# Kernel tuning notes

Hardware: AMD Instinct MI355X
Metric: run time of the kernel (lower is better)

## Reference

```python
import jax, jax.numpy as jnp
import numpy as np

B = 1024
NUM_DENSE = 13
NUM_SPARSE = 26
VOCAB = 100000
EMB_DIM = 16
BOT = [512, 256, 64, 16]
TOP = [1024, 512, 256]
D_INT = BOT[-1] + NUM_SPARSE * EMB_DIM  # 432
OUT_INT = D_INT * (D_INT + 1) // 2      # 93528


def setup_inputs() -> dict:
    key = jax.random.key(0)
    ks = jax.random.split(key, 32)
    inp = {
        "dense_features": jax.random.normal(ks[0], (B, NUM_DENSE), jnp.float32),
        "sparse_features": jax.random.randint(ks[1], (B, NUM_SPARSE), 0, VOCAB),
        "emb_tables": jax.random.normal(ks[2], (NUM_SPARSE, VOCAB, EMB_DIM), jnp.float32) * 0.02,
    }
    # bottom MLP weights (in, out) convention
    dims = [NUM_DENSE] + BOT
    for i in range(len(BOT)):
        inp[f"bw{i}"] = jax.random.normal(ks[3 + i], (dims[i], dims[i + 1]), jnp.float32) * 0.02
        inp[f"bb{i}"] = jnp.zeros((dims[i + 1],), jnp.float32)
    tdims = [BOT[-1] + OUT_INT] + TOP + [1]
    for i in range(len(TOP) + 1):
        inp[f"tw{i}"] = jax.random.normal(ks[10 + i], (tdims[i], tdims[i + 1]), jnp.float32) * 0.02
        inp[f"tb{i}"] = jnp.zeros((tdims[i + 1],), jnp.float32)
    return inp


def _forward(dense_features, emb_tables, bws, bbs, tws, tbs, sparse_features):
    # bottom MLP: Linear+ReLU stacks
    h = dense_features
    for w, b in zip(bws, bbs):
        h = jax.nn.relu(h @ w + b)
    dense_out = h  # (B, 16)
    # embedding lookups: table t indexed by column t of sparse_features
    # emb_tables: (F, V, E); gather per-table then flatten -> (B, F*E)
    emb = jnp.take_along_axis(
        emb_tables[None],  # (1, F, V, E)
        sparse_features.T[None, :, :, None].transpose(0, 1, 2, 3) * 0 + sparse_features.T[None, :, :, None],
        axis=2,
    )  # placeholder avoided below
    # cleaner: vmap over tables
    emb = jax.vmap(lambda tbl, idx: tbl[idx], in_axes=(0, 1))(emb_tables, sparse_features)  # (F, B, E)
    emb = jnp.transpose(emb, (1, 0, 2)).reshape(dense_features.shape[0], -1)  # (B, F*E)
    x = jnp.concatenate([dense_out, emb], axis=1)  # (B, D_INT)
    # pairwise interaction: upper triangle (incl. diagonal) of outer product.
    iu0, iu1 = np.triu_indices(x.shape[1])
    inter = x[:, iu0] * x[:, iu1]  # (B, OUT_INT) -- only needed entries
    z = jnp.concatenate([dense_out, inter], axis=1)
    n_top = len(tws)
    for i, (w, b) in enumerate(zip(tws, tbs)):
        z = z @ w + b
        if i < n_top - 1:
            z = jax.nn.relu(z)
    return z


def reference(dense_features, sparse_features, emb_tables,
              bw0, bb0, bw1, bb1, bw2, bb2, bw3, bb3,
              tw0, tb0, tw1, tb1, tw2, tb2, tw3, tb3):
    bws = [bw0, bw1, bw2, bw3]
    bbs = [bb0, bb1, bb2, bb3]
    tws = [tw0, tw1, tw2, tw3]
    tbs = [tb0, tb1, tb2, tb3]
    return _forward(dense_features, emb_tables, bws, bbs, tws, tbs, sparse_features)
```

## Files before the change

### kernel.cpp

```cpp
#include <hip/hip_runtime.h>
#include <stdint.h>

typedef unsigned short ushort_t;
typedef __attribute__((ext_vector_type(4))) float f32x4;
typedef __attribute__((ext_vector_type(8))) short s16x8;

#define DEVFN static __device__ __forceinline__

constexpr int B_   = 1024;
constexpr int P_   = 93528;
constexpr int K1   = 93544;
constexpr int Kp   = 94208;
constexpr int SPLITS = 16;
constexpr int KCH  = Kp / SPLITS;
constexpr int KSTEPS = KCH / 64;

DEVFN ushort_t f2bf(float f) {
  union { float f; unsigned int u; } x; x.f = f;
  unsigned int r = x.u + 0x7FFFu + ((x.u >> 16) & 1u);
  return (ushort_t)(r >> 16);
}

DEVFN void gload_lds16(const void* g, void* l) {
  __builtin_amdgcn_global_load_lds((const __attribute__((address_space(1))) unsigned int*)g,
                                   (__attribute__((address_space(3))) unsigned int*)l, 16, 0, 0);
}

__global__ __launch_bounds__(256) void k_pre(const float* __restrict__ dense,
    const int* __restrict__ sparse, const float* __restrict__ tbl,
    const float* __restrict__ bw0, const float* __restrict__ bb0,
    const float* __restrict__ bw1, const float* __restrict__ bb1,
    const float* __restrict__ bw2, const float* __restrict__ bb2,
    const float* __restrict__ bw3, const float* __restrict__ bb3,
    int* __restrict__ iu, float* __restrict__ xT) {
  __shared__ float sm[13520];
  int bid = blockIdx.x, t = threadIdx.x;
  if (bid < 368) {
    int k = bid * 256 + t;
    if (bid < 8) {
      int idx = bid * 256 + t;
      xT[432 * 1024 + idx] = (idx < 1024) ? 1.f : 0.f;
    }
    if (k >= Kp) return;
    int v;
    if (k < 16) v = k | (432 << 16);
    else if (k >= K1) v = 433 | (433 << 16);
    else {
      int p = k - 16;
      float s = sqrtf((float)(748225 - 8 * p));
      int i = (int)((865.0f - s) * 0.5f);
      if (i < 0) i = 0; if (i > 431) i = 431;
      while (i < 431 && (i + 1) * (865 - (i + 1)) / 2 <= p) ++i;
      while (i > 0 && i * (865 - i) / 2 > p) --i;
      int j = i + (p - i * (865 - i) / 2);
      v = i | (j << 16);
    }
    iu[k] = v;
  } else if (bid < 432) {
    float* xs = sm;
    float* h1 = sm + 208;
    float* h2 = h1 + 8192;
    float* h3 = h2 + 4096;
    int m0 = (bid - 368) * 16;
    if (t < 208) xs[t] = dense[m0 * 13 + t];
    __syncthreads();
    #pragma unroll
    for (int h = 0; h < 2; ++h) {
      int n = h * 256 + t;
      float a[16];
      float bv = bb0[n];
      #pragma unroll
      for (int r = 0; r < 16; ++r) a[r] = bv;
      for (int k = 0; k < 13; ++k) {
        float w = bw0[k * 512 + n];
        #pragma unroll
        for (int r = 0; r < 16; ++r) a[r] = fmaf(xs[r * 13 + k], w, a[r]);
      }
      #pragma unroll
      for (int r = 0; r < 16; ++r) h1[r * 512 + n] = fmaxf(a[r], 0.f);
    }
    __syncthreads();
    {
      int n = t;
      float a[16];
      float bv = bb1[n];
      #pragma unroll
      for (int r = 0; r < 16; ++r) a[r] = bv;
      for (int k = 0; k < 512; ++k) {
        float w = bw1[k * 256 + n];
        #pragma unroll
        for (int r = 0; r < 16; ++r) a[r] = fmaf(h1[r * 512 + k], w, a[r]);
      }
      #pragma unroll
      for (int r = 0; r < 16; ++r) h2[r * 256 + n] = fmaxf(a[r], 0.f);
    }
    __syncthreads();
    {
      int n = t & 63, r0 = t >> 6;
      float a[4];
      float bv = bb2[n];
      #pragma unroll
      for (int i = 0; i < 4; ++i) a[i] = bv;
      for (int k = 0; k < 256; ++k) {
        float w = bw2[k * 64 + n];
        #pragma unroll
        for (int i = 0; i < 4; ++i) a[i] = fmaf(h2[(r0 + 4 * i) * 256 + k], w, a[i]);
      }
      #pragma unroll
      for (int i = 0; i < 4; ++i) h3[(r0 + 4 * i) * 64 + n] = fmaxf(a[i], 0.f);
    }
    __syncthreads();
    {
      int n = t & 15, r = t >> 4;
      float a = bb3[n];
      for (int k = 0; k < 64; ++k) a = fmaf(h3[r * 64 + k], bw3[k * 16 + n], a);
      xT[(size_t)n * B_ + m0 + r] = fmaxf(a, 0.f);
    }
  } else {
    int e = bid - 432;
    int f = e >> 2;
    int b = (e & 3) * 256 + t;
    int idx = sparse[(size_t)b * 26 + f];
    const float4* src = (const float4*)(tbl + ((size_t)f * 100000 + idx) * 16);
    #pragma unroll
    for (int q = 0; q < 4; ++q) {
      float4 v = src[q];
      int r = 16 + f * 16 + q * 4;
      xT[(size_t)(r + 0) * B_ + b] = v.x;
      xT[(size_t)(r + 1) * B_ + b] = v.y;
      xT[(size_t)(r + 2) * B_ + b] = v.z;
      xT[(size_t)(r + 3) * B_ + b] = v.w;
    }
  }
}

__global__ __launch_bounds__(256, 8) void k_gz(const float* __restrict__ xT,
                                               const int* __restrict__ iu,
                                               const float* __restrict__ tw0,
                                               ushort_t* __restrict__ Z,
                                               ushort_t* __restrict__ WT) {
  __shared__ int ls_iu[512];
  int bid = blockIdx.x, t = threadIdx.x;
  int r3 = bid % 3;
  if (r3 == 0) {
    int idx = bid / 3;
    int l = t & 63, w = t >> 6;
    int mb = (idx & 15) * 64;
    int kt = (idx >> 4) * 512;
    ls_iu[t] = iu[kt + t];
    ls_iu[256 + t] = iu[kt + 256 + t];
    __syncthreads();
    uint32_t moff = mb + l;
    int kw = w * 128;
    #pragma unroll 2
    for (int g = 0; g < 16; ++g) {
      int kloc = kw + g * 8;
      int4 ij0 = *(const int4*)&ls_iu[kloc];
      int4 ij1 = *(const int4*)&ls_iu[kloc + 4];
      float p[8];
      {
        int v0 = ij0.x, v1 = ij0.y, v2 = ij0.z, v3 = ij0.w;
        p[0] = xT[(uint32_t)((v0 & 0xFFFF) << 10) + moff] * xT[(uint32_t)((v0 >> 16) << 10) + moff];
        p[1] = xT[(uint32_t)((v1 & 0xFFFF) << 10) + moff] * xT[(uint32_t)((v1 >> 16) << 10) + moff];
        p[2] = xT[(uint32_t)((v2 & 0xFFFF) << 10) + moff] * xT[(uint32_t)((v2 >> 16) << 10) + moff];
        p[3] = xT[(uint32_t)((v3 & 0xFFFF) << 10) + moff] * xT[(uint32_t)((v3 >> 16) << 10) + moff];
        v0 = ij1.x; v1 = ij1.y; v2 = ij1.z; v3 = ij1.w;
        p[4] = xT[(uint32_t)((v0 & 0xFFFF) << 10) + moff] * xT[(uint32_t)((v0 >> 16) << 10) + moff];
        p[5] = xT[(uint32_t)((v1 & 0xFFFF) << 10) + moff] * xT[(uint32_t)((v1 >> 16) << 10) + moff];
        p[6] = xT[(uint32_t)((v2 & 0xFFFF) << 10) + moff] * xT[(uint32_t)((v2 >> 16) << 10) + moff];
        p[7] = xT[(uint32_t)((v3 & 0xFFFF) << 10) + moff] * xT[(uint32_t)((v3 >> 16) << 10) + moff];
      }
      union { uint32_t w4[4]; int4 v4; } o;
      asm("v_cvt_pk_bf16_f32 %0, %1, %2" : "=v"(o.w4[0]) : "v"(p[0]), "v"(p[1]));
      asm("v_cvt_pk_bf16_f32 %0, %1, %2" : "=v"(o.w4[1]) : "v"(p[2]), "v"(p[3]));
      asm("v_cvt_pk_bf16_f32 %0, %1, %2" : "=v"(o.w4[2]) : "v"(p[4]), "v"(p[5]));
      asm("v_cvt_pk_bf16_f32 %0, %1, %2" : "=v"(o.w4[3]) : "v"(p[6]), "v"(p[7]));
      int kglob = kt + kloc;
      *(int4*)&Z[((size_t)(kglob >> 3) * 1024 + moff) * 8] = o.v4;
    }
  } else {
    int idx = (bid / 3) * 2 + r3 - 1;
    int k0 = (idx % 368) * 256, n0 = (idx / 368) * 64;
    int nl = t & 63, kq = t >> 6;
    int n = n0 + nl;
    int kbase = k0 + kq * 64;
    const float* src = tw0 + (size_t)kbase * 1024 + n;
    ushort_t* dst = WT + ((size_t)(kbase >> 3) * 1024 + n) * 8;
    bool full = (kbase + 64 <= K1);
    #pragma unroll
    for (int g = 0; g < 8; ++g) {
      float v[8];
      if (full) {
        #pragma unroll
        for (int e = 0; e < 8; ++e) v[e] = src[(size_t)(g * 8 + e) << 10];
      } else {
        #pragma unroll
        for (int e = 0; e < 8; ++e) {
          int k = kbase + g * 8 + e;
          v[e] = (k < K1) ? src[(size_t)(g * 8 + e) << 10] : 0.f;
        }
      }
      union { uint32_t w4[4]; int4 v4; } o;
      asm("v_cvt_pk_bf16_f32 %0, %1, %2" : "=v"(o.w4[0]) : "v"(v[0]), "v"(v[1]));
      asm("v_cvt_pk_bf16_f32 %0, %1, %2" : "=v"(o.w4[1]) : "v"(v[2]), "v"(v[3]));
      asm("v_cvt_pk_bf16_f32 %0, %1, %2" : "=v"(o.w4[2]) : "v"(v[4]), "v"(v[5]));
      asm("v_cvt_pk_bf16_f32 %0, %1, %2" : "=v"(o.w4[3]) : "v"(v[6]), "v"(v[7]));
      *(int4*)(dst + (size_t)g * 8192) = o.v4;
    }
  }
}

__global__ __launch_bounds__(512, 2) void k_gemm(const ushort_t* __restrict__ Z,
                                                 const ushort_t* __restrict__ WT,
                                                 float* __restrict__ part) {
  __shared__ ushort_t lds[65536];
  int t = threadIdx.x;
  int bid = blockIdx.x;
  int x = bid & 7, r = bid >> 3;
  int g = (x << 3) | (r & 7);
  int s = g >> 2;
  int m0 = (g & 3) * 256, n0 = (r >> 3) * 256;
  int kb = s * KCH;

  int rr = t >> 3, cc = t & 7;
  int cs = cc ^ (rr & 7);
  const ushort_t* pa0 = Z  + (((size_t)(kb >> 3) + cs) * 1024 + m0 + rr) * 8;
  const ushort_t* pb0 = WT + (((size_t)(kb >> 3) + cs) * 1024 + n0 + rr) * 8;
  int l0 = t * 8;

  int w = t >> 6, l = t & 63;
  int wm = (w >> 2) * 128, wn = (w & 3) * 64;
  int lhi = l >> 4, llo = l & 15;

  f32x4 acc[8][4];
  #pragma unroll
  for (int a = 0; a < 8; ++a)
    #pragma unroll
    for (int b = 0; b < 4; ++b) acc[a][b] = f32x4{0.f, 0.f, 0.f, 0.f};

  s16x8 bf[4][2], afX[4], afY[4];

  auto rdA = [&](s16x8* dst, int mfb, const ushort_t* Ab) {
    #pragma unroll
    for (int j = 0; j < 2; ++j)
      #pragma unroll
      for (int ks = 0; ks < 2; ++ks) {
        int row = wm + (mfb + j) * 16 + llo;
        int ch = (ks * 4 + lhi) ^ (row & 7);
        dst[j * 2 + ks] = *(const s16x8*)&Ab[row * 64 + ch * 8];
      }
  };
  auto rdB = [&](const ushort_t* Bb) {
    #pragma unroll
    for (int nf = 0; nf < 4; ++nf)
      #pragma unroll
      for (int ks = 0; ks < 2; ++ks) {
        int row = wn + nf * 16 + llo;
        int ch = (ks * 4 + lhi) ^ (row & 7);
        bf[nf][ks] = *(const s16x8*)&Bb[row * 64 + ch * 8];
      }
  };

#define MFMA_PHASE(P, AF)                                                        \
  __builtin_amdgcn_s_barrier();                                                  \
  asm volatile("s_waitcnt lgkmcnt(0)" ::: "memory");                             \
  __builtin_amdgcn_sched_barrier(0);                                             \
  __builtin_amdgcn_s_setprio(1);                                                 \
  _Pragma("unroll")                                                              \
  for (int j = 0; j < 2; ++j)                                                    \
    _Pragma("unroll")                                                            \
    for (int nf = 0; nf < 4; ++nf)                                               \
      _Pragma("unroll")                                                          \
      for (int ks = 0; ks < 2; ++ks)                                             \
        acc[(P) * 2 + j][nf] = __builtin_amdgcn_mfma_f32_16x16x32_bf16(          \
            AF[j * 2 + ks], bf[nf][ks], acc[(P) * 2 + j][nf], 0, 0, 0);          \
  __builtin_amdgcn_s_setprio(0);                                                 \
  __builtin_amdgcn_sched_barrier(0);                                             \
  __builtin_amdgcn_s_barrier();

  #pragma unroll
  for (int i = 0; i < 4; ++i) gload_lds16(pa0 + i * 512, &lds[i * 4096 + l0]);
  #pragma unroll
  for (int i = 0; i < 4; ++i) gload_lds16(pb0 + i * 512, &lds[32768 + i * 4096 + l0]);
  #pragma unroll
  for (int i = 0; i < 4; ++i) gload_lds16(pb0 + 65536 + i * 512, &lds[32768 + 16384 + i * 4096 + l0]);
  asm volatile("s_waitcnt vmcnt(4)" ::: "memory");
  __builtin_amdgcn_s_barrier();
  rdA(afX, 0, &lds[0]);

  for (int tt = 0; tt < KSTEPS; ++tt) {
    const ushort_t* Ab = &lds[(tt & 1) * 16384];
    const ushort_t* An = &lds[((tt + 1) & 1) * 16384];
    const ushort_t* Bb = &lds[32768 + (tt & 1) * 16384];
    ushort_t* dA  = &lds[((tt + 1) & 1) * 16384];
    ushort_t* dB2 = &lds[32768 + (tt & 1) * 16384];
    const ushort_t* sA  = pa0 + (size_t)(tt + 1) * 65536;
    const ushort_t* sB2 = pb0 + (size_t)(tt + 2) * 65536;
    bool pf1 = (tt + 1 < KSTEPS);
    bool pf2 = (tt + 2 < KSTEPS);

    rdB(Bb);
    rdA(afY, 2, Ab);
    if (pf1) {
      gload_lds16(sA,       dA + l0);
      gload_lds16(sA + 512, dA + 4096 + l0);
    }
    MFMA_PHASE(0, afX)

    rdA(afX, 4, Ab);
    if (pf1) {
      gload_lds16(sA + 1024, dA + 2 * 4096 + l0);
      gload_lds16(sA + 1536, dA + 3 * 4096 + l0);
    }
    MFMA_PHASE(1, afY)

    rdA(afY, 6, Ab);
    if (pf2) {
      gload_lds16(sB2,       dB2 + l0);
      gload_lds16(sB2 + 512, dB2 + 4096 + l0);
    }
    MFMA_PHASE(2, afX)

    if (pf1) {
      if (pf2) asm volatile("s_waitcnt vmcnt(2)" ::: "memory");
      else     asm volatile("s_waitcnt vmcnt(0)" ::: "memory");
      rdA(afX, 0, An);
    }
    if (pf2) {
      gload_lds16(sB2 + 1024, dB2 + 2 * 4096 + l0);
      gload_lds16(sB2 + 1536, dB2 + 3 * 4096 + l0);
    }
    MFMA_PHASE(3, afY)
  }
#undef MFMA_PHASE

  float* pbase = part + ((size_t)s << 20);
  #pragma unroll
  for (int mf = 0; mf < 8; ++mf)
    #pragma unroll
    for (int nf = 0; nf < 4; ++nf) {
      int n = n0 + wn + nf * 16 + llo;
      #pragma unroll
      for (int r2 = 0; r2 < 4; ++r2) {
        int m = m0 + wm + mf * 16 + lhi * 4 + r2;
        pbase[(size_t)m * 1024 + n] = acc[mf][nf][r2];
      }
    }
}

__global__ __launch_bounds__(256) void k_red(const float* __restrict__ part,
                                             const float* __restrict__ bias,
                                             float* __restrict__ z1) {
  int idx = blockIdx.x * 256 + threadIdx.x;
  float a = bias[idx & 1023];
  #pragma unroll
  for (int s = 0; s < SPLITS; ++s) a += part[((size_t)s << 20) + idx];
  z1[idx] = fmaxf(a, 0.f);
}

template<int K, int N>
__global__ __launch_bounds__(256) void k_sgemm(const float* __restrict__ A,
                                               const float* __restrict__ W,
                                               const float* __restrict__ bias,
                                               float* __restrict__ C) {
  __shared__ float As[16][34];
  __shared__ float Bs[16][68];
  int t = threadIdx.x;
  int m0 = blockIdx.x * 32, n0 = blockIdx.y * 64;
  int tx = t & 15, ty = t >> 4;
  float acc[2][4];
  #pragma unroll
  for (int j = 0; j < 2; ++j)
    #pragma unroll
    for (int q = 0; q < 4; ++q) acc[j][q] = 0.f;
  int ar = t >> 3, ak = (t & 7) * 2;
  int bk = t >> 4, bn = (t & 15) * 4;
  for (int k0 = 0; k0 < K; k0 += 16) {
    float2 av = *(const float2*)&A[(size_t)(m0 + ar) * K + k0 + ak];
    float4 bv = *(const float4*)&W[(size_t)(k0 + bk) * N + n0 + bn];
    __syncthreads();
    As[ak][ar] = av.x; As[ak + 1][ar] = av.y;
    *(float4*)&Bs[bk][bn] = bv;
    __syncthreads();
    #pragma unroll
    for (int k = 0; k < 16; ++k) {
      float2 a = *(const float2*)&As[k][ty * 2];
      float4 b = *(const float4*)&Bs[k][tx * 4];
      acc[0][0] = fmaf(a.x, b.x, acc[0][0]); acc[0][1] = fmaf(a.x, b.y, acc[0][1]);
      acc[0][2] = fmaf(a.x, b.z, acc[0][2]); acc[0][3] = fmaf(a.x, b.w, acc[0][3]);
      acc[1][0] = fmaf(a.y, b.x, acc[1][0]); acc[1][1] = fmaf(a.y, b.y, acc[1][1]);
      acc[1][2] = fmaf(a.y, b.z, acc[1][2]); acc[1][3] = fmaf(a.y, b.w, acc[1][3]);
    }
  }
  #pragma unroll
  for (int j = 0; j < 2; ++j) {
    int m = m0 + ty * 2 + j;
    float4 o;
    o.x = fmaxf(acc[j][0] + bias[n0 + tx * 4 + 0], 0.f);
    o.y = fmaxf(acc[j][1] + bias[n0 + tx * 4 + 1], 0.f);
    o.z = fmaxf(acc[j][2] + bias[n0 + tx * 4 + 2], 0.f);
    o.w = fmaxf(acc[j][3] + bias[n0 + tx * 4 + 3], 0.f);
    *(float4*)&C[(size_t)m * N + n0 + tx * 4] = o;
  }
}

__global__ __launch_bounds__(256) void k_last(const float* __restrict__ z3,
                                              const float* __restrict__ w,
                                              const float* __restrict__ bias,
                                              float* __restrict__ out) {
  int t = threadIdx.x, l = t & 63, wv = t >> 6;
  int m = blockIdx.x * 4 + wv;
  float s = 0.f;
  #pragma unroll
  for (int c = 0; c < 4; ++c) s = fmaf(z3[(size_t)m * 256 + c * 64 + l], w[c * 64 + l], s);
  #pragma unroll
  for (int off = 32; off; off >>= 1) s += __shfl_down(s, off, 64);
  if (l == 0) out[m] = s + bias[0];
}

__global__ __launch_bounds__(256) void k_z1init(const float* __restrict__ bias, float* __restrict__ z1) {
  int idx = blockIdx.x * 256 + threadIdx.x;
  z1[idx] = bias[idx & 1023];
}
__global__ __launch_bounds__(256) void k_relu(float* __restrict__ z1) {
  int idx = blockIdx.x * 256 + threadIdx.x;
  z1[idx] = fmaxf(z1[idx], 0.f);
}
constexpr int FB_S = 8;
__global__ __launch_bounds__(256) void k_fbgemm(const float* __restrict__ xT,
                                                const int* __restrict__ iu,
                                                const float* __restrict__ tw0,
                                                float* __restrict__ z1) {
  __shared__ float zs[32 * 64];
  __shared__ float wsb[32 * 64];
  int t = threadIdx.x;
  int m0 = blockIdx.x * 64, n0 = blockIdx.y * 64, s = blockIdx.z;
  int kch = (K1 + FB_S - 1) / FB_S;
  int k0 = s * kch, kend = min(k0 + kch, K1);
  float acc[16];
  #pragma unroll
  for (int q = 0; q < 16; ++q) acc[q] = 0.f;
  int mm = t & 63, ng = t >> 6;
  for (int kk = k0; kk < kend; kk += 32) {
    __syncthreads();
    for (int sl = t; sl < 2048; sl += 256) {
      int kloc = sl >> 6, v6 = sl & 63;
      int k = kk + kloc;
      float zv = 0.f, wv = 0.f;
      if (k < kend) {
        int ij = iu[k];
        int i = ij & 0xFFFF, j = ij >> 16;
        zv = xT[(size_t)i * B_ + m0 + v6] * xT[(size_t)j * B_ + m0 + v6];
        wv = tw0[(size_t)k * 1024 + n0 + v6];
      }
      zs[kloc * 64 + v6] = zv;
      wsb[kloc * 64 + v6] = wv;
    }
    __syncthreads();
    #pragma unroll 4
    for (int kloc = 0; kloc < 32; ++kloc) {
      float zv = zs[kloc * 64 + mm];
      #pragma unroll
      for (int q = 0; q < 16; ++q)
        acc[q] = fmaf(zv, wsb[kloc * 64 + ng * 16 + q], acc[q]);
    }
  }
  #pragma unroll
  for (int q = 0; q < 16; ++q)
    atomicAdd(&z1[(size_t)(m0 + mm) * 1024 + n0 + ng * 16 + q], acc[q]);
}

extern "C" void kernel_launch(void* const* d_in, const int* in_sizes, int n_in,
                              void* d_out, int out_size, void* d_ws, size_t ws_size,
                              hipStream_t stream) {
  const float* dense  = (const float*)d_in[0];
  const int*   sparse = (const int*)  d_in[1];
  const float* emb    = (const float*)d_in[2];
  const float* bw0 = (const float*)d_in[3];  const float* bb0 = (const float*)d_in[4];
  const float* bw1 = (const float*)d_in[5];  const float* bb1 = (const float*)d_in[6];
  const float* bw2 = (const float*)d_in[7];  const float* bb2 = (const float*)d_in[8];
  const float* bw3 = (const float*)d_in[9];  const float* bb3 = (const float*)d_in[10];
  const float* tw0 = (const float*)d_in[11]; const float* tb0 = (const float*)d_in[12];
  const float* tw1 = (const float*)d_in[13]; const float* tb1 = (const float*)d_in[14];
  const float* tw2 = (const float*)d_in[15]; const float* tb2 = (const float*)d_in[16];
  const float* tw3 = (const float*)d_in[17]; const float* tb3 = (const float*)d_in[18];
  float* out = (float*)d_out;

  char* ws = (char*)d_ws;
  size_t off = 0;
  auto alloc = [&](size_t bytes) -> char* {
    char* p = ws + off;
    off = (off + bytes + 255) & ~(size_t)255;
    return p;
  };
  float* xT = (float*)alloc((size_t)434 * 1024 * 4);
  int*   iu = (int*)  alloc((size_t)Kp * 4);
  float* z1 = (float*)alloc((size_t)1024 * 1024 * 4);
  float* z2 = (float*)alloc((size_t)1024 * 512 * 4);
  float* z3 = (float*)alloc((size_t)1024 * 256 * 4);
  ushort_t* Z    = (ushort_t*)alloc((size_t)1024 * Kp * 2);
  ushort_t* WT   = (ushort_t*)alloc((size_t)1024 * Kp * 2);
  float*    part = (float*)   alloc((size_t)SPLITS * 1024 * 1024 * 4);
  bool big = (off <= ws_size);

  k_pre<<<536, 256, 0, stream>>>(dense, sparse, emb, bw0, bb0, bw1, bb1, bw2, bb2, bw3, bb3, iu, xT);

  if (big) {
    k_gz<<<8832, 256, 0, stream>>>(xT, iu, tw0, Z, WT);
    k_gemm<<<256, 512, 0, stream>>>(Z, WT, part);
    k_red<<<4096, 256, 0, stream>>>(part, tb0, z1);
  } else {
    k_z1init<<<4096, 256, 0, stream>>>(tb0, z1);
    k_fbgemm<<<dim3(16, 16, FB_S), 256, 0, stream>>>(xT, iu, tw0, z1);
    k_relu<<<4096, 256, 0, stream>>>(z1);
  }

  k_sgemm<1024, 512><<<dim3(32, 8), 256, 0, stream>>>(z1, tw1, tb1, z2);
  k_sgemm<512, 256><<<dim3(32, 4), 256, 0, stream>>>(z2, tw2, tb2, z3);
  k_last<<<256, 256, 0, stream>>>(z3, tw3, tb3, out);
}
```

Measured before the change: 530.3 us.

## Move tw0 bf16 conversion into pre kernel and split bottom MLP finer

The fp32-to-bf16 transposed conversion of tw0 moves from the Z-generation kernel into the preprocessing kernel, because it depends only on weights. It then runs alongside the bottom MLP, embedding gather and index-table work, and Z generation becomes its own smaller kernel. The bottom MLP now uses 256 blocks of 4 rows each instead of 64 blocks of 16, which spreads that long serial chain across more CUs and shrinks shared memory. In exchange the pre kernel gets a very large grid that mixes heterogeneous work, and the MLP blocks reread the weights more often.

```diff
diff --git a/kernel.cpp b/kernel.cpp
--- a/kernel.cpp
+++ b/kernel.cpp
@@ -32,13 +32,70 @@
     const float* __restrict__ bw1, const float* __restrict__ bb1,
     const float* __restrict__ bw2, const float* __restrict__ bb2,
     const float* __restrict__ bw3, const float* __restrict__ bb3,
-    int* __restrict__ iu, float* __restrict__ xT) {
-  __shared__ float sm[13520];
+    const float* __restrict__ tw0,
+    int* __restrict__ iu, float* __restrict__ xT, ushort_t* __restrict__ WT) {
+  __shared__ float sm[3392];
   int bid = blockIdx.x, t = threadIdx.x;
-  if (bid < 368) {
-    int k = bid * 256 + t;
-    if (bid < 8) {
-      int idx = bid * 256 + t;
+  if (bid < 256) {
+    float* xs = sm;
+    float* h1 = sm + 64;
+    float* h2 = h1 + 2048;
+    float* h3 = h2 + 1024;
+    int m0 = bid * 4;
+    if (t < 52) xs[t] = dense[m0 * 13 + t];
+    __syncthreads();
+    #pragma unroll
+    for (int h = 0; h < 2; ++h) {
+      int n = h * 256 + t;
+      float a[4];
+      float bv = bb0[n];
+      #pragma unroll
+      for (int r = 0; r < 4; ++r) a[r] = bv;
+      for (int k = 0; k < 13; ++k) {
+        float w = bw0[k * 512 + n];
+        #pragma unroll
+        for (int r = 0; r < 4; ++r) a[r] = fmaf(xs[r * 13 + k], w, a[r]);
+      }
+      #pragma unroll
+      for (int r = 0; r < 4; ++r) h1[r * 512 + n] = fmaxf(a[r], 0.f);
+    }
+    __syncthreads();
+    {
+      int n = t;
+      float a[4];
+      float bv = bb1[n];
+      #pragma unroll
+      for (int r = 0; r < 4; ++r) a[r] = bv;
+      #pragma unroll 8
+      for (int k = 0; k < 512; ++k) {
+        float w = bw1[k * 256 + n];
+        #pragma unroll
+        for (int r = 0; r < 4; ++r) a[r] = fmaf(h1[r * 512 + k], w, a[r]);
+      }
+      #pragma unroll
+      for (int r = 0; r < 4; ++r) h2[r * 256 + n] = fmaxf(a[r], 0.f);
+    }
+    __syncthreads();
+    {
+      int n = t & 63, r = t >> 6;
+      float a = bb2[n];
+      #pragma unroll 8
+      for (int k = 0; k < 256; ++k) a = fmaf(h2[r * 256 + k], bw2[k * 64 + n], a);
+      h3[r * 64 + n] = fmaxf(a, 0.f);
+    }
+    __syncthreads();
+    if (t < 64) {
+      int n = t & 15, r = t >> 4;
+      float a = bb3[n];
+      #pragma unroll 8
+      for (int k = 0; k < 64; ++k) a = fmaf(h3[r * 64 + k], bw3[k * 16 + n], a);
+      xT[(size_t)n * B_ + m0 + r] = fmaxf(a, 0.f);
+    }
+  } else if (bid < 624) {
+    int bb = bid - 256;
+    int k = bb * 256 + t;
+    if (bb < 8) {
+      int idx = bb * 256 + t;
       xT[432 * 1024 + idx] = (idx < 1024) ? 1.f : 0.f;
     }
     if (k >= Kp) return;
@@ -56,68 +113,8 @@
       v = i | (j << 16);
     }
     iu[k] = v;
-  } else if (bid < 432) {
-    float* xs = sm;
-    float* h1 = sm + 208;
-    float* h2 = h1 + 8192;
-    float* h3 = h2 + 4096;
-    int m0 = (bid - 368) * 16;
-    if (t < 208) xs[t] = dense[m0 * 13 + t];
-    __syncthreads();
-    #pragma unroll
-    for (int h = 0; h < 2; ++h) {
-      int n = h * 256 + t;
-      float a[16];
-      float bv = bb0[n];
-      #pragma unroll
-      for (int r = 0; r < 16; ++r) a[r] = bv;
-      for (int k = 0; k < 13; ++k) {
-        float w = bw0[k * 512 + n];
-        #pragma unroll
-        for (int r = 0; r < 16; ++r) a[r] = fmaf(xs[r * 13 + k], w, a[r]);
-      }
-      #pragma unroll
-      for (int r = 0; r < 16; ++r) h1[r * 512 + n] = fmaxf(a[r], 0.f);
-    }
-    __syncthreads();
-    {
-      int n = t;
-      float a[16];
-      float bv = bb1[n];
-      #pragma unroll
-      for (int r = 0; r < 16; ++r) a[r] = bv;
-      for (int k = 0; k < 512; ++k) {
-        float w = bw1[k * 256 + n];
-        #pragma unroll
-        for (int r = 0; r < 16; ++r) a[r] = fmaf(h1[r * 512 + k], w, a[r]);
-      }
-      #pragma unroll
-      for (int r = 0; r < 16; ++r) h2[r * 256 + n] = fmaxf(a[r], 0.f);
-    }
-    __syncthreads();
-    {
-      int n = t & 63, r0 = t >> 6;
-      float a[4];
-      float bv = bb2[n];
-      #pragma unroll
-      for (int i = 0; i < 4; ++i) a[i] = bv;
-      for (int k = 0; k < 256; ++k) {
-        float w = bw2[k * 64 + n];
-        #pragma unroll
-        for (int i = 0; i < 4; ++i) a[i] = fmaf(h2[(r0 + 4 * i) * 256 + k], w, a[i]);
-      }
-      #pragma unroll
-      for (int i = 0; i < 4; ++i) h3[(r0 + 4 * i) * 64 + n] = fmaxf(a[i], 0.f);
-    }
-    __syncthreads();
-    {
-      int n = t & 15, r = t >> 4;
-      float a = bb3[n];
-      for (int k = 0; k < 64; ++k) a = fmaf(h3[r * 64 + k], bw3[k * 16 + n], a);
-      xT[(size_t)n * B_ + m0 + r] = fmaxf(a, 0.f);
-    }
-  } else {
-    int e = bid - 432;
+  } else if (bid < 728) {
+    int e = bid - 624;
     int f = e >> 2;
     int b = (e & 3) * 256 + t;
     int idx = sparse[(size_t)b * 26 + f];
@@ -131,55 +128,8 @@
       xT[(size_t)(r + 2) * B_ + b] = v.z;
       xT[(size_t)(r + 3) * B_ + b] = v.w;
     }
-  }
-}
-
-__global__ __launch_bounds__(256, 8) void k_gz(const float* __restrict__ xT,
-                                               const int* __restrict__ iu,
-                                               const float* __restrict__ tw0,
-                                               ushort_t* __restrict__ Z,
-                                               ushort_t* __restrict__ WT) {
-  __shared__ int ls_iu[512];
-  int bid = blockIdx.x, t = threadIdx.x;
-  int r3 = bid % 3;
-  if (r3 == 0) {
-    int idx = bid / 3;
-    int l = t & 63, w = t >> 6;
-    int mb = (idx & 15) * 64;
-    int kt = (idx >> 4) * 512;
-    ls_iu[t] = iu[kt + t];
-    ls_iu[256 + t] = iu[kt + 256 + t];
-    __syncthreads();
-    uint32_t moff = mb + l;
-    int kw = w * 128;
-    #pragma unroll 2
-    for (int g = 0; g < 16; ++g) {
-      int kloc = kw + g * 8;
-      int4 ij0 = *(const int4*)&ls_iu[kloc];
-      int4 ij1 = *(const int4*)&ls_iu[kloc + 4];
-      float p[8];
-      {
-        int v0 = ij0.x, v1 = ij0.y, v2 = ij0.z, v3 = ij0.w;
-        p[0] = xT[(uint32_t)((v0 & 0xFFFF) << 10) + moff] * xT[(uint32_t)((v0 >> 16) << 10) + moff];
-        p[1] = xT[(uint32_t)((v1 & 0xFFFF) << 10) + moff] * xT[(uint32_t)((v1 >> 16) << 10) + moff];
-        p[2] = xT[(uint32_t)((v2 & 0xFFFF) << 10) + moff] * xT[(uint32_t)((v2 >> 16) << 10) + moff];
-        p[3] = xT[(uint32_t)((v3 & 0xFFFF) << 10) + moff] * xT[(uint32_t)((v3 >> 16) << 10) + moff];
-        v0 = ij1.x; v1 = ij1.y; v2 = ij1.z; v3 = ij1.w;
-        p[4] = xT[(uint32_t)((v0 & 0xFFFF) << 10) + moff] * xT[(uint32_t)((v0 >> 16) << 10) + moff];
-        p[5] = xT[(uint32_t)((v1 & 0xFFFF) << 10) + moff] * xT[(uint32_t)((v1 >> 16) << 10) + moff];
-        p[6] = xT[(uint32_t)((v2 & 0xFFFF) << 10) + moff] * xT[(uint32_t)((v2 >> 16) << 10) + moff];
-        p[7] = xT[(uint32_t)((v3 & 0xFFFF) << 10) + moff] * xT[(uint32_t)((v3 >> 16) << 10) + moff];
-      }
-      union { uint32_t w4[4]; int4 v4; } o;
-      asm("v_cvt_pk_bf16_f32 %0, %1, %2" : "=v"(o.w4[0]) : "v"(p[0]), "v"(p[1]));
-      asm("v_cvt_pk_bf16_f32 %0, %1, %2" : "=v"(o.w4[1]) : "v"(p[2]), "v"(p[3]));
-      asm("v_cvt_pk_bf16_f32 %0, %1, %2" : "=v"(o.w4[2]) : "v"(p[4]), "v"(p[5]));
-      asm("v_cvt_pk_bf16_f32 %0, %1, %2" : "=v"(o.w4[3]) : "v"(p[6]), "v"(p[7]));
-      int kglob = kt + kloc;
-      *(int4*)&Z[((size_t)(kglob >> 3) * 1024 + moff) * 8] = o.v4;
-    }
   } else {
-    int idx = (bid / 3) * 2 + r3 - 1;
+    int idx = bid - 728;
     int k0 = (idx % 368) * 256, n0 = (idx / 368) * 64;
     int nl = t & 63, kq = t >> 6;
     int n = n0 + nl;
@@ -207,6 +157,47 @@
       asm("v_cvt_pk_bf16_f32 %0, %1, %2" : "=v"(o.w4[3]) : "v"(v[6]), "v"(v[7]));
       *(int4*)(dst + (size_t)g * 8192) = o.v4;
     }
+  }
+}
+
+__global__ __launch_bounds__(256, 8) void k_genz(const float* __restrict__ xT,
+                                                 const int* __restrict__ iu,
+                                                 ushort_t* __restrict__ Z) {
+  __shared__ int ls_iu[512];
+  int idx = blockIdx.x, t = threadIdx.x;
+  int l = t & 63, w = t >> 6;
+  int mb = (idx & 15) * 64;
+  int kt = (idx >> 4) * 512;
+  ls_iu[t] = iu[kt + t];
+  ls_iu[256 + t] = iu[kt + 256 + t];
+  __syncthreads();
+  uint32_t moff = mb + l;
+  int kw = w * 128;
+  #pragma unroll 2
+  for (int g = 0; g < 16; ++g) {
+    int kloc = kw + g * 8;
+    int4 ij0 = *(const int4*)&ls_iu[kloc];
+    int4 ij1 = *(const int4*)&ls_iu[kloc + 4];
+    float p[8];
+    {
+      int v0 = ij0.x, v1 = ij0.y, v2 = ij0.z, v3 = ij0.w;
+      p[0] = xT[(uint32_t)((v0 & 0xFFFF) << 10) + moff] * xT[(uint32_t)((v0 >> 16) << 10) + moff];
+      p[1] = xT[(uint32_t)((v1 & 0xFFFF) << 10) + moff] * xT[(uint32_t)((v1 >> 16) << 10) + moff];
+      p[2] = xT[(uint32_t)((v2 & 0xFFFF) << 10) + moff] * xT[(uint32_t)((v2 >> 16) << 10) + moff];
+      p[3] = xT[(uint32_t)((v3 & 0xFFFF) << 10) + moff] * xT[(uint32_t)((v3 >> 16) << 10) + moff];
+      v0 = ij1.x; v1 = ij1.y; v2 = ij1.z; v3 = ij1.w;
+      p[4] = xT[(uint32_t)((v0 & 0xFFFF) << 10) + moff] * xT[(uint32_t)((v0 >> 16) << 10) + moff];
+      p[5] = xT[(uint32_t)((v1 & 0xFFFF) << 10) + moff] * xT[(uint32_t)((v1 >> 16) << 10) + moff];
+      p[6] = xT[(uint32_t)((v2 & 0xFFFF) << 10) + moff] * xT[(uint32_t)((v2 >> 16) << 10) + moff];
+      p[7] = xT[(uint32_t)((v3 & 0xFFFF) << 10) + moff] * xT[(uint32_t)((v3 >> 16) << 10) + moff];
+    }
+    union { uint32_t w4[4]; int4 v4; } o;
+    asm("v_cvt_pk_bf16_f32 %0, %1, %2" : "=v"(o.w4[0]) : "v"(p[0]), "v"(p[1]));
+    asm("v_cvt_pk_bf16_f32 %0, %1, %2" : "=v"(o.w4[1]) : "v"(p[2]), "v"(p[3]));
+    asm("v_cvt_pk_bf16_f32 %0, %1, %2" : "=v"(o.w4[2]) : "v"(p[4]), "v"(p[5]));
+    asm("v_cvt_pk_bf16_f32 %0, %1, %2" : "=v"(o.w4[3]) : "v"(p[6]), "v"(p[7]));
+    int kglob = kt + kloc;
+    *(int4*)&Z[((size_t)(kglob >> 3) * 1024 + moff) * 8] = o.v4;
   }
 }
 
@@ -503,10 +494,12 @@
   float*    part = (float*)   alloc((size_t)SPLITS * 1024 * 1024 * 4);
   bool big = (off <= ws_size);
 
-  k_pre<<<536, 256, 0, stream>>>(dense, sparse, emb, bw0, bb0, bw1, bb1, bw2, bb2, bw3, bb3, iu, xT);
+  int preGrid = big ? 6616 : 728;
+  k_pre<<<preGrid, 256, 0, stream>>>(dense, sparse, emb, bw0, bb0, bw1, bb1,
+                                     bw2, bb2, bw3, bb3, tw0, iu, xT, WT);
 
   if (big) {
-    k_gz<<<8832, 256, 0, stream>>>(xT, iu, tw0, Z, WT);
+    k_genz<<<2944, 256, 0, stream>>>(xT, iu, Z);
     k_gemm<<<256, 512, 0, stream>>>(Z, WT, part);
     k_red<<<4096, 256, 0, stream>>>(part, tb0, z1);
   } else {
```

After: 479.2 us. 9.6% less time.
